# Kernel optimization log

Hardware: AMD Instinct MI355X
Metric: run time of the kernel (lower is better)

Reference implementation:

```python
import jax, jax.numpy as jnp
import numpy as np

WEIGHT = 1.0
BIN_SIZE = 1.0
MAX_MZ = 2000.0
NUM_BINS = int(MAX_MZ / BIN_SIZE)  # 2000
B, N = 8192, 256


def setup_inputs() -> dict:
    key = jax.random.key(0)
    k1, k2, k3, k4, k5 = jax.random.split(key, 5)
    return {
        "pred_mz": jax.random.uniform(k1, (B, N), dtype=jnp.float32),
        "pred_intensity": jax.random.uniform(k2, (B, N), dtype=jnp.float32),
        "target_mz": jax.random.uniform(k3, (B, N), dtype=jnp.float32),
        "target_intensity": jax.random.uniform(k4, (B, N), dtype=jnp.float32),
        "target_mask": jax.random.uniform(k5, (B, N), dtype=jnp.float32),
    }


def _bin_spectrum(mz, intensity):
    # mz is normalized to [0,1]; denormalize and bin. Batched scatter-add:
    # a single 2D indexed add replaces the per-sample scatter_add_ loop.
    bin_idx = jnp.clip((mz * MAX_MZ / BIN_SIZE).astype(jnp.int32), 0, NUM_BINS - 1)  # [B, N]
    bsz = mz.shape[0]
    binned = jnp.zeros((bsz, NUM_BINS), dtype=intensity.dtype)
    return binned.at[jnp.arange(bsz)[:, None], bin_idx].add(intensity)


def reference(pred_mz, pred_intensity, target_mz, target_intensity, target_mask):
    pred_binned = _bin_spectrum(pred_mz, pred_intensity)                    # [B, NUM_BINS]
    target_binned = _bin_spectrum(target_mz, target_intensity * target_mask)
    eps = 1e-8  # matches torch F.cosine_similarity default
    pn = jnp.maximum(jnp.linalg.norm(pred_binned, axis=1), eps)
    tn = jnp.maximum(jnp.linalg.norm(target_binned, axis=1), eps)
    cos = jnp.sum(pred_binned * target_binned, axis=1) / (pn * tn)
    cos = jnp.clip(cos, -1.0, 1.0)
    angle = jnp.arccos(cos)
    loss = jnp.mean(angle / jnp.pi)
    return WEIGHT * loss
```

## Files before the change

### kernel.cpp

```cpp
#include <hip/hip_runtime.h>
#include <math.h>


#define SAL_NUM_BINS 2000
#define SAL_B 8192
#define SAL_N 256

__global__ __launch_bounds__(256) void sal_row_kernel(
    const float* __restrict__ pred_mz,
    const float* __restrict__ pred_int,
    const float* __restrict__ targ_mz,
    const float* __restrict__ targ_int,
    const float* __restrict__ targ_mask,
    float* __restrict__ row_angle)
{
    __shared__ float ph[SAL_NUM_BINS];
    __shared__ float th[SAL_NUM_BINS];
    const int b = blockIdx.x;
    const int t = threadIdx.x;

    for (int i = t; i < SAL_NUM_BINS; i += 256) { ph[i] = 0.0f; th[i] = 0.0f; }
    __syncthreads();

    const int base = b * SAL_N;
    {
        float pmz = pred_mz[base + t];
        float pin = pred_int[base + t];
        float tmz = targ_mz[base + t];
        float tin = targ_int[base + t] * targ_mask[base + t];
        int pb = (int)(pmz * 2000.0f);
        pb = min(max(pb, 0), SAL_NUM_BINS - 1);
        int tb = (int)(tmz * 2000.0f);
        tb = min(max(tb, 0), SAL_NUM_BINS - 1);
        atomicAdd(&ph[pb], pin);
        atomicAdd(&th[tb], tin);
    }
    __syncthreads();

    float dot = 0.0f, p2 = 0.0f, t2 = 0.0f;
    for (int i = t; i < SAL_NUM_BINS; i += 256) {
        float p = ph[i], q = th[i];
        dot = fmaf(p, q, dot);
        p2  = fmaf(p, p, p2);
        t2  = fmaf(q, q, t2);
    }

    for (int off = 32; off > 0; off >>= 1) {
        dot += __shfl_down(dot, off, 64);
        p2  += __shfl_down(p2,  off, 64);
        t2  += __shfl_down(t2,  off, 64);
    }
    __shared__ float rbuf[3][4];
    const int wave = t >> 6;
    const int lane = t & 63;
    if (lane == 0) { rbuf[0][wave] = dot; rbuf[1][wave] = p2; rbuf[2][wave] = t2; }
    __syncthreads();
    if (t == 0) {
        float d = rbuf[0][0] + rbuf[0][1] + rbuf[0][2] + rbuf[0][3];
        float a = rbuf[1][0] + rbuf[1][1] + rbuf[1][2] + rbuf[1][3];
        float c = rbuf[2][0] + rbuf[2][1] + rbuf[2][2] + rbuf[2][3];
        float pn = fmaxf(sqrtf(a), 1e-8f);
        float tn = fmaxf(sqrtf(c), 1e-8f);
        float cs = d / (pn * tn);
        cs = fminf(fmaxf(cs, -1.0f), 1.0f);
        row_angle[b] = acosf(cs) * (float)(1.0 / M_PI);
    }
}

__global__ __launch_bounds__(256) void sal_reduce_kernel(
    const float* __restrict__ row_angle, float* __restrict__ out)
{
    const int t = threadIdx.x;
    float s = 0.0f;
    for (int i = t; i < SAL_B; i += 256) s += row_angle[i];
    for (int off = 32; off > 0; off >>= 1) s += __shfl_down(s, off, 64);
    __shared__ float rbuf[4];
    const int wave = t >> 6;
    const int lane = t & 63;
    if (lane == 0) rbuf[wave] = s;
    __syncthreads();
    if (t == 0) out[0] = (rbuf[0] + rbuf[1] + rbuf[2] + rbuf[3]) * (float)(1.0 / SAL_B);
}

extern "C" void kernel_launch(void* const* d_in, const int* in_sizes, int n_in,
                              void* d_out, int out_size, void* d_ws, size_t ws_size,
                              hipStream_t stream) {
    const float* pred_mz   = (const float*)d_in[0];
    const float* pred_int  = (const float*)d_in[1];
    const float* targ_mz   = (const float*)d_in[2];
    const float* targ_int  = (const float*)d_in[3];
    const float* targ_mask = (const float*)d_in[4];
    float* row_angle = (float*)d_ws;
    float* out = (float*)d_out;

    sal_row_kernel<<<SAL_B, 256, 0, stream>>>(pred_mz, pred_int, targ_mz,
                                              targ_int, targ_mask, row_angle);
    sal_reduce_kernel<<<1, 256, 0, stream>>>(row_angle, out);
}
```

Before: 122.5 us.

## Process two rows per block with vectorized loads and float4 histogram reduction

Each 256-thread block now handles two spectra, with 128 threads per row each loading float2 elements and doing two atomic adds per histogram. Histogram zeroing and the dot/norm reduction use float4 shared-memory accesses, and the final reduce kernel reads row angles as float4. The goal is to halve the block count and cut per-block fixed overhead such as zeroing and syncs relative to useful work, and to reduce instruction count. In exchange each block uses twice the LDS (32KB), which may limit occupancy.

```diff
diff --git a/kernel.cpp b/kernel.cpp
--- a/kernel.cpp
+++ b/kernel.cpp
@@ -5,6 +5,8 @@
 #define SAL_NUM_BINS 2000
 #define SAL_B 8192
 #define SAL_N 256
+#define SAL_RPB 2
+#define SAL_BLOCKS (SAL_B / SAL_RPB)
 
 __global__ __launch_bounds__(256) void sal_row_kernel(
     const float* __restrict__ pred_mz,
@@ -14,35 +16,51 @@
     const float* __restrict__ targ_mask,
     float* __restrict__ row_angle)
 {
-    __shared__ float ph[SAL_NUM_BINS];
-    __shared__ float th[SAL_NUM_BINS];
-    const int b = blockIdx.x;
+    __shared__ __align__(16) float hist[SAL_RPB][2][SAL_NUM_BINS];
+    __shared__ float rbuf[SAL_RPB][2][3];
     const int t = threadIdx.x;
 
-    for (int i = t; i < SAL_NUM_BINS; i += 256) { ph[i] = 0.0f; th[i] = 0.0f; }
-    __syncthreads();
-
-    const int base = b * SAL_N;
     {
-        float pmz = pred_mz[base + t];
-        float pin = pred_int[base + t];
-        float tmz = targ_mz[base + t];
-        float tin = targ_int[base + t] * targ_mask[base + t];
-        int pb = (int)(pmz * 2000.0f);
-        pb = min(max(pb, 0), SAL_NUM_BINS - 1);
-        int tb = (int)(tmz * 2000.0f);
-        tb = min(max(tb, 0), SAL_NUM_BINS - 1);
-        atomicAdd(&ph[pb], pin);
-        atomicAdd(&th[tb], tin);
+        float4* h4 = (float4*)&hist[0][0][0];
+        const float4 z = make_float4(0.f, 0.f, 0.f, 0.f);
+        #pragma unroll
+        for (int i = 0; i < 8; ++i) {
+            int idx = t + i * 256;
+            if (idx < (SAL_RPB * 2 * SAL_NUM_BINS) / 4) h4[idx] = z;
+        }
     }
     __syncthreads();
 
-    float dot = 0.0f, p2 = 0.0f, t2 = 0.0f;
-    for (int i = t; i < SAL_NUM_BINS; i += 256) {
-        float p = ph[i], q = th[i];
-        dot = fmaf(p, q, dot);
-        p2  = fmaf(p, p, p2);
-        t2  = fmaf(q, q, t2);
+    const int r   = t >> 7;
+    const int u   = t & 127;
+    const int row = blockIdx.x * SAL_RPB + r;
+    const int base = row * SAL_N;
+
+    const float2 pmz = ((const float2*)(pred_mz  + base))[u];
+    const float2 pin = ((const float2*)(pred_int + base))[u];
+    const float2 tmz = ((const float2*)(targ_mz  + base))[u];
+    const float2 tin = ((const float2*)(targ_int + base))[u];
+    const float2 tms = ((const float2*)(targ_mask+ base))[u];
+
+    int pb0 = min(max((int)(pmz.x * 2000.0f), 0), SAL_NUM_BINS - 1);
+    int pb1 = min(max((int)(pmz.y * 2000.0f), 0), SAL_NUM_BINS - 1);
+    int tb0 = min(max((int)(tmz.x * 2000.0f), 0), SAL_NUM_BINS - 1);
+    int tb1 = min(max((int)(tmz.y * 2000.0f), 0), SAL_NUM_BINS - 1);
+    atomicAdd(&hist[r][0][pb0], pin.x);
+    atomicAdd(&hist[r][0][pb1], pin.y);
+    atomicAdd(&hist[r][1][tb0], tin.x * tms.x);
+    atomicAdd(&hist[r][1][tb1], tin.y * tms.y);
+    __syncthreads();
+
+    const float4* p4 = (const float4*)&hist[r][0][0];
+    const float4* q4 = (const float4*)&hist[r][1][0];
+    float dot = 0.f, p2 = 0.f, t2 = 0.f;
+    for (int i = u; i < SAL_NUM_BINS / 4; i += 128) {
+        float4 p = p4[i], q = q4[i];
+        dot = fmaf(p.x, q.x, dot); p2 = fmaf(p.x, p.x, p2); t2 = fmaf(q.x, q.x, t2);
+        dot = fmaf(p.y, q.y, dot); p2 = fmaf(p.y, p.y, p2); t2 = fmaf(q.y, q.y, t2);
+        dot = fmaf(p.z, q.z, dot); p2 = fmaf(p.z, p.z, p2); t2 = fmaf(q.z, q.z, t2);
+        dot = fmaf(p.w, q.w, dot); p2 = fmaf(p.w, p.w, p2); t2 = fmaf(q.w, q.w, t2);
     }
 
     for (int off = 32; off > 0; off >>= 1) {
@@ -50,20 +68,20 @@
         p2  += __shfl_down(p2,  off, 64);
         t2  += __shfl_down(t2,  off, 64);
     }
-    __shared__ float rbuf[3][4];
-    const int wave = t >> 6;
-    const int lane = t & 63;
-    if (lane == 0) { rbuf[0][wave] = dot; rbuf[1][wave] = p2; rbuf[2][wave] = t2; }
+    const int wir = (t >> 6) & 1;
+    if ((t & 63) == 0) {
+        rbuf[r][wir][0] = dot; rbuf[r][wir][1] = p2; rbuf[r][wir][2] = t2;
+    }
     __syncthreads();
-    if (t == 0) {
-        float d = rbuf[0][0] + rbuf[0][1] + rbuf[0][2] + rbuf[0][3];
-        float a = rbuf[1][0] + rbuf[1][1] + rbuf[1][2] + rbuf[1][3];
-        float c = rbuf[2][0] + rbuf[2][1] + rbuf[2][2] + rbuf[2][3];
+    if (u == 0) {
+        float d = rbuf[r][0][0] + rbuf[r][1][0];
+        float a = rbuf[r][0][1] + rbuf[r][1][1];
+        float c = rbuf[r][0][2] + rbuf[r][1][2];
         float pn = fmaxf(sqrtf(a), 1e-8f);
         float tn = fmaxf(sqrtf(c), 1e-8f);
         float cs = d / (pn * tn);
         cs = fminf(fmaxf(cs, -1.0f), 1.0f);
-        row_angle[b] = acosf(cs) * (float)(1.0 / M_PI);
+        row_angle[row] = acosf(cs) * (float)(1.0 / M_PI);
     }
 }
 
@@ -71,15 +89,18 @@
     const float* __restrict__ row_angle, float* __restrict__ out)
 {
     const int t = threadIdx.x;
+    const float4* ra4 = (const float4*)row_angle;
     float s = 0.0f;
-    for (int i = t; i < SAL_B; i += 256) s += row_angle[i];
+    for (int i = t; i < SAL_B / 4; i += 256) {
+        float4 v = ra4[i];
+        s += (v.x + v.y) + (v.z + v.w);
+    }
     for (int off = 32; off > 0; off >>= 1) s += __shfl_down(s, off, 64);
     __shared__ float rbuf[4];
     const int wave = t >> 6;
-    const int lane = t & 63;
-    if (lane == 0) rbuf[wave] = s;
+    if ((t & 63) == 0) rbuf[wave] = s;
     __syncthreads();
-    if (t == 0) out[0] = (rbuf[0] + rbuf[1] + rbuf[2] + rbuf[3]) * (float)(1.0 / SAL_B);
+    if (t == 0) out[0] = ((rbuf[0] + rbuf[1]) + (rbuf[2] + rbuf[3])) * (float)(1.0 / SAL_B);
 }
 
 extern "C" void kernel_launch(void* const* d_in, const int* in_sizes, int n_in,
@@ -93,7 +114,7 @@
     float* row_angle = (float*)d_ws;
     float* out = (float*)d_out;
 
-    sal_row_kernel<<<SAL_B, 256, 0, stream>>>(pred_mz, pred_int, targ_mz,
-                                              targ_int, targ_mask, row_angle);
+    sal_row_kernel<<<SAL_BLOCKS, 256, 0, stream>>>(pred_mz, pred_int, targ_mz,
+                                                   targ_int, targ_mask, row_angle);
     sal_reduce_kernel<<<1, 256, 0, stream>>>(row_angle, out);
 }
```

Result: faster. 112.5 us (-8.2%).

## Use one wavefront per row and compute norms by gathering from histogram bins

Applied to the files above, without the earlier changes.

Each 64-lane wavefront now processes one spectrum row with float4 loads and builds a private LDS histogram, so block-level barriers are no longer needed. The dot product and squared norms are computed as sums over input elements of intensity times the histogram value at that element's bin. This replaces the scan over all 2000 bins and relies on the identity sum_bins p*q = sum_i p_i*q[bin_i]. It costs four times more LDS per block, about 64KB, which limits how many blocks fit per CU. The final reduction kernel is also vectorized with float4 loads.

```diff
diff --git a/kernel.cpp b/kernel.cpp
--- a/kernel.cpp
+++ b/kernel.cpp
@@ -14,56 +14,72 @@
     const float* __restrict__ targ_mask,
     float* __restrict__ row_angle)
 {
-    __shared__ float ph[SAL_NUM_BINS];
-    __shared__ float th[SAL_NUM_BINS];
-    const int b = blockIdx.x;
+    __shared__ __align__(16) float hist[4][2][SAL_NUM_BINS];
     const int t = threadIdx.x;
+    const int w = t >> 6;
+    const int l = t & 63;
+    const int row = blockIdx.x * 4 + w;
+    const int base = row * SAL_N;
 
-    for (int i = t; i < SAL_NUM_BINS; i += 256) { ph[i] = 0.0f; th[i] = 0.0f; }
-    __syncthreads();
+    const float4 pmz = ((const float4*)(pred_mz   + base))[l];
+    const float4 pin = ((const float4*)(pred_int  + base))[l];
+    const float4 tmz = ((const float4*)(targ_mz   + base))[l];
+    const float4 ti4 = ((const float4*)(targ_int  + base))[l];
+    const float4 tm4 = ((const float4*)(targ_mask + base))[l];
 
-    const int base = b * SAL_N;
     {
-        float pmz = pred_mz[base + t];
-        float pin = pred_int[base + t];
-        float tmz = targ_mz[base + t];
-        float tin = targ_int[base + t] * targ_mask[base + t];
-        int pb = (int)(pmz * 2000.0f);
-        pb = min(max(pb, 0), SAL_NUM_BINS - 1);
-        int tb = (int)(tmz * 2000.0f);
-        tb = min(max(tb, 0), SAL_NUM_BINS - 1);
-        atomicAdd(&ph[pb], pin);
-        atomicAdd(&th[tb], tin);
-    }
-    __syncthreads();
-
-    float dot = 0.0f, p2 = 0.0f, t2 = 0.0f;
-    for (int i = t; i < SAL_NUM_BINS; i += 256) {
-        float p = ph[i], q = th[i];
-        dot = fmaf(p, q, dot);
-        p2  = fmaf(p, p, p2);
-        t2  = fmaf(q, q, t2);
+        float4* h4 = (float4*)&hist[w][0][0];
+        const float4 z = make_float4(0.f, 0.f, 0.f, 0.f);
+        #pragma unroll
+        for (int i = 0; i < 16; ++i) {
+            int idx = l + i * 64;
+            if (idx < (2 * SAL_NUM_BINS) / 4) h4[idx] = z;
+        }
     }
 
+    const float tinx = ti4.x * tm4.x, tiny_ = ti4.y * tm4.y;
+    const float tinz = ti4.z * tm4.z, tinw = ti4.w * tm4.w;
+
+    const int pb0 = min(max((int)(pmz.x * 2000.0f), 0), SAL_NUM_BINS - 1);
+    const int pb1 = min(max((int)(pmz.y * 2000.0f), 0), SAL_NUM_BINS - 1);
+    const int pb2 = min(max((int)(pmz.z * 2000.0f), 0), SAL_NUM_BINS - 1);
+    const int pb3 = min(max((int)(pmz.w * 2000.0f), 0), SAL_NUM_BINS - 1);
+    const int tb0 = min(max((int)(tmz.x * 2000.0f), 0), SAL_NUM_BINS - 1);
+    const int tb1 = min(max((int)(tmz.y * 2000.0f), 0), SAL_NUM_BINS - 1);
+    const int tb2 = min(max((int)(tmz.z * 2000.0f), 0), SAL_NUM_BINS - 1);
+    const int tb3 = min(max((int)(tmz.w * 2000.0f), 0), SAL_NUM_BINS - 1);
+
+    atomicAdd(&hist[w][0][pb0], pin.x);
+    atomicAdd(&hist[w][0][pb1], pin.y);
+    atomicAdd(&hist[w][0][pb2], pin.z);
+    atomicAdd(&hist[w][0][pb3], pin.w);
+    atomicAdd(&hist[w][1][tb0], tinx);
+    atomicAdd(&hist[w][1][tb1], tiny_);
+    atomicAdd(&hist[w][1][tb2], tinz);
+    atomicAdd(&hist[w][1][tb3], tinw);
+
+    float dot = 0.f, p2 = 0.f, t2 = 0.f;
+    dot = fmaf(pin.x, hist[w][1][pb0], dot);  p2 = fmaf(pin.x, hist[w][0][pb0], p2);
+    dot = fmaf(pin.y, hist[w][1][pb1], dot);  p2 = fmaf(pin.y, hist[w][0][pb1], p2);
+    dot = fmaf(pin.z, hist[w][1][pb2], dot);  p2 = fmaf(pin.z, hist[w][0][pb2], p2);
+    dot = fmaf(pin.w, hist[w][1][pb3], dot);  p2 = fmaf(pin.w, hist[w][0][pb3], p2);
+    t2  = fmaf(tinx, hist[w][1][tb0], t2);
+    t2  = fmaf(tiny_, hist[w][1][tb1], t2);
+    t2  = fmaf(tinz, hist[w][1][tb2], t2);
+    t2  = fmaf(tinw, hist[w][1][tb3], t2);
+
+    #pragma unroll
     for (int off = 32; off > 0; off >>= 1) {
         dot += __shfl_down(dot, off, 64);
         p2  += __shfl_down(p2,  off, 64);
         t2  += __shfl_down(t2,  off, 64);
     }
-    __shared__ float rbuf[3][4];
-    const int wave = t >> 6;
-    const int lane = t & 63;
-    if (lane == 0) { rbuf[0][wave] = dot; rbuf[1][wave] = p2; rbuf[2][wave] = t2; }
-    __syncthreads();
-    if (t == 0) {
-        float d = rbuf[0][0] + rbuf[0][1] + rbuf[0][2] + rbuf[0][3];
-        float a = rbuf[1][0] + rbuf[1][1] + rbuf[1][2] + rbuf[1][3];
-        float c = rbuf[2][0] + rbuf[2][1] + rbuf[2][2] + rbuf[2][3];
-        float pn = fmaxf(sqrtf(a), 1e-8f);
-        float tn = fmaxf(sqrtf(c), 1e-8f);
-        float cs = d / (pn * tn);
+    if (l == 0) {
+        float pn = fmaxf(sqrtf(p2), 1e-8f);
+        float tn = fmaxf(sqrtf(t2), 1e-8f);
+        float cs = dot / (pn * tn);
         cs = fminf(fmaxf(cs, -1.0f), 1.0f);
-        row_angle[b] = acosf(cs) * (float)(1.0 / M_PI);
+        row_angle[row] = acosf(cs) * (float)(1.0 / M_PI);
     }
 }
 
@@ -71,15 +87,19 @@
     const float* __restrict__ row_angle, float* __restrict__ out)
 {
     const int t = threadIdx.x;
+    const float4* ra4 = (const float4*)row_angle;
     float s = 0.0f;
-    for (int i = t; i < SAL_B; i += 256) s += row_angle[i];
+    #pragma unroll
+    for (int i = 0; i < SAL_B / 4 / 256; ++i) {
+        float4 v = ra4[t + i * 256];
+        s += (v.x + v.y) + (v.z + v.w);
+    }
+    #pragma unroll
     for (int off = 32; off > 0; off >>= 1) s += __shfl_down(s, off, 64);
     __shared__ float rbuf[4];
-    const int wave = t >> 6;
-    const int lane = t & 63;
-    if (lane == 0) rbuf[wave] = s;
+    if ((t & 63) == 0) rbuf[t >> 6] = s;
     __syncthreads();
-    if (t == 0) out[0] = (rbuf[0] + rbuf[1] + rbuf[2] + rbuf[3]) * (float)(1.0 / SAL_B);
+    if (t == 0) out[0] = ((rbuf[0] + rbuf[1]) + (rbuf[2] + rbuf[3])) * (float)(1.0 / SAL_B);
 }
 
 extern "C" void kernel_launch(void* const* d_in, const int* in_sizes, int n_in,
@@ -93,7 +113,7 @@
     float* row_angle = (float*)d_ws;
     float* out = (float*)d_out;
 
-    sal_row_kernel<<<SAL_B, 256, 0, stream>>>(pred_mz, pred_int, targ_mz,
-                                              targ_int, targ_mask, row_angle);
+    sal_row_kernel<<<SAL_B / 4, 256, 0, stream>>>(pred_mz, pred_int, targ_mz,
+                                                  targ_int, targ_mask, row_angle);
     sal_reduce_kernel<<<1, 256, 0, stream>>>(row_angle, out);
 }
```

Measured after the change: 108.4 us. 11.6% less time.
